# Performance work log

Hardware: AMD Instinct MI355X
Metric: run time of the kernel (lower is better)

Reference implementation:

```python
import jax, jax.numpy as jnp
import numpy as np

K = 512
D = 512
N_D = 4
SUB_D = D // N_D  # 128
B, T = 16, 2048
TAU = 2.0


def setup_inputs() -> dict:
    key = jax.random.key(0)
    kx, kw1, kw2, kw3, kw4, kg = jax.random.split(key, 6)
    x = jax.random.normal(kx, (B, D, T), dtype=jnp.float32)
    scale = 1.0 / K
    def init_w(k):
        return jax.random.uniform(k, (K, SUB_D), dtype=jnp.float32, minval=-scale, maxval=scale)
    W1, W2, W3, W4 = init_w(kw1), init_w(kw2), init_w(kw3), init_w(kw4)
    # Standard Gumbel noise g = -log(-log(U)), fixed here for reproducibility
    u = jax.random.uniform(kg, (N_D, B * T, K), dtype=jnp.float32, minval=1e-10, maxval=1.0)
    gumbels = -jnp.log(-jnp.log(u))
    return {"x": x, "W1": W1, "W2": W2, "W3": W3, "W4": W4, "gumbels": gumbels}


def reference(x, W1, W2, W3, W4, gumbels):
    # x: [B, D, T] -> [B, T, D] -> flat [N, D] -> [n_d, N, sub_D]
    Bv, Dv, Tv = x.shape
    flat = jnp.transpose(x, (0, 2, 1)).reshape(-1, Dv)          # [N, D]
    xg = jnp.transpose(flat.reshape(-1, N_D, SUB_D), (1, 0, 2))  # [n_d, N, sub_D]
    W = jnp.stack([W1, W2, W3, W4], axis=0)                      # [n_d, K, sub_D]

    code_sqr = jnp.sum(W * W, axis=-1)                           # [n_d, K]
    in_sqr = jnp.sum(xg * xg, axis=-1, keepdims=True)            # [n_d, N, 1]
    cross = jnp.einsum('gnd,gkd->gnk', xg, W)                    # [n_d, N, K]
    dis = code_sqr[:, None, :] + in_sqr - 2.0 * cross            # [n_d, N, K]

    # gumbel_softmax(-dis, tau, hard=False): softmax((logits + g)/tau)
    enc = jax.nn.softmax((-dis + gumbels) / TAU, axis=-1)        # [n_d, N, K]

    quant = jnp.einsum('gnk,gkd->gnd', enc, W)                   # [n_d, N, sub_D]
    quant = jnp.transpose(quant, (1, 0, 2)).reshape(Bv, Tv, Dv)  # concat sub-dims
    quant = jnp.transpose(quant, (0, 2, 1))                      # [B, D, T]

    avg_probs = jnp.mean(enc, axis=1)                            # [n_d, K]
    perp = jnp.sum(jnp.exp(-jnp.sum(avg_probs * jnp.log(avg_probs + 1e-10), axis=-1)))
    return quant, perp
```

## Files before the change

kernel.cpp:

```cpp
#include <hip/hip_runtime.h>
#include <hip/hip_bf16.h>
#include <math.h>

#define K_CODES 512
#define D_FULL 512
#define SUB_D 128
#define N_D 4
#define B_SZ 16
#define T_SZ 2048
#define N_TOK (B_SZ * T_SZ)
#define TILE 32
#define QS_STRIDE 33

typedef __attribute__((ext_vector_type(8))) short short8;
typedef __attribute__((ext_vector_type(16))) float f32x16;

__device__ __forceinline__ unsigned short f2bf(float f) {
    __hip_bfloat16 h = __float2bfloat16(f);
    return *reinterpret_cast<unsigned short*>(&h);
}
__device__ __forceinline__ float bf2f(unsigned short u) {
    unsigned int v = ((unsigned int)u) << 16;
    return __uint_as_float(v);
}

#define XS_OFF  32768
#define SMEM_SZ 40960

__device__ __forceinline__ int enc_idx(int r, int c) { return r * 512 + (c ^ ((r & 7) << 3)); }
__device__ __forceinline__ int xs_idx(int t, int d)  { return t * 128 + (d ^ ((t & 7) << 3)); }

__global__ __launch_bounds__(256, 4) void vq_kernel(
    const float* __restrict__ x,
    const unsigned short* __restrict__ Wbf,
    const unsigned short* __restrict__ WTbf,
    const float* __restrict__ csqr,
    const float* __restrict__ gum,
    float* __restrict__ out,
    float* __restrict__ wsum, int Rmask)
{
    __shared__ __align__(16) char smem[SMEM_SZ];
    unsigned short* enc = (unsigned short*)smem;
    unsigned short* xs  = (unsigned short*)(smem + XS_OFF);
    float* Sp   = (float*)smem;
    float* Qs   = (float*)smem;

    const int tid = threadIdx.x;
    const int g = blockIdx.y;
    const int n0 = blockIdx.x * TILE;
    const int b = n0 / T_SZ;
    const int t0 = n0 % T_SZ;
    const int wave = tid >> 6, lane = tid & 63;
    const int half = lane >> 5, l31 = lane & 31;

    const float* xbase = x + ((size_t)b * D_FULL + g * SUB_D) * T_SZ + t0;
    #pragma unroll
    for (int it = 0; it < 4; ++it) {
        int idx = tid + it * 256;
        int tq = idx & 7, d = idx >> 3;
        float4 v = *(const float4*)(xbase + (size_t)d * T_SZ + tq * 4);
        int t = tq * 4;
        xs[xs_idx(t + 0, d)] = f2bf(v.x);
        xs[xs_idx(t + 1, d)] = f2bf(v.y);
        xs[xs_idx(t + 2, d)] = f2bf(v.z);
        xs[xs_idx(t + 3, d)] = f2bf(v.w);
    }
    __syncthreads();

    float csq[4];
    #pragma unroll
    for (int ct = 0; ct < 4; ++ct)
        csq[ct] = csqr[g * K_CODES + wave * 128 + ct * 32 + l31];

    const unsigned short* Wg = Wbf + (size_t)g * K_CODES * SUB_D;
    f32x16 acc[4];
    #pragma unroll
    for (int ct = 0; ct < 4; ++ct)
        #pragma unroll
        for (int i = 0; i < 16; ++i) acc[ct][i] = 0.f;

    #pragma unroll
    for (int s = 0; s < 8; ++s) {
        short8 af = *(const short8*)(xs + xs_idx(l31, s * 16 + half * 8));
        #pragma unroll
        for (int ct = 0; ct < 4; ++ct) {
            short8 bfrag = *(const short8*)(Wg + (size_t)(wave * 128 + ct * 32 + l31) * SUB_D
                                            + s * 16 + half * 8);
            acc[ct] = __builtin_amdgcn_mfma_f32_32x32x16_bf16(af, bfrag, acc[ct], 0, 0, 0);
        }
    }

    __builtin_amdgcn_sched_barrier(0);

    const float* gw = gum + ((size_t)g * N_TOK + n0) * K_CODES + wave * 128;
    float4 f[16];
    #pragma unroll
    for (int k = 0; k < 16; ++k)
        f[k] = *(const float4*)(gw + (size_t)(2 * k + half) * K_CODES + 4 * l31);

    float* Sw = Sp + wave * 544;
    float ssum[16];
    #pragma unroll
    for (int i = 0; i < 16; ++i) ssum[i] = 0.f;

    #pragma unroll
    for (int j = 0; j < 8; ++j) {
        *(float4*)(Sw + half * 128 + 4 * l31)       = f[2 * j];
        *(float4*)(Sw + 256 + half * 128 + 4 * l31) = f[2 * j + 1];
        int hj = j & 1;
        if (half == hj) {
            int q = (j - hj) >> 1;
            #pragma unroll
            for (int ct = 0; ct < 4; ++ct)
                #pragma unroll
                for (int m = 0; m < 4; ++m) {
                    float gv = Sw[m * 128 + ct * 32 + l31];
                    int i = q * 4 + m;
                    float e = __expf(acc[ct][i] - 0.5f * csq[ct] + 0.5f * gv);
                    acc[ct][i] = e;
                    ssum[i] += e;
                }
        }
    }

    #pragma unroll
    for (int i = 0; i < 16; ++i) {
        float s = ssum[i];
        s += __shfl_xor(s, 1);  s += __shfl_xor(s, 2);
        s += __shfl_xor(s, 4);  s += __shfl_xor(s, 8);
        s += __shfl_xor(s, 16);
        ssum[i] = s;
    }
    if (l31 == 0) {
        #pragma unroll
        for (int i = 0; i < 16; ++i)
            Sw[512 + (i & 3) + 8 * (i >> 2) + 4 * half] = ssum[i];
    }
    __syncthreads();

    float rinv[16];
    #pragma unroll
    for (int i = 0; i < 16; ++i) {
        int r = (i & 3) + 8 * (i >> 2) + 4 * half;
        float s = Sp[512 + r] + Sp[544 + 512 + r] + Sp[1088 + 512 + r] + Sp[1632 + 512 + r];
        rinv[i] = 1.f / s;
    }
    __syncthreads();

    float* wrep = wsum + (size_t)(blockIdx.x & Rmask) * (N_D * K_CODES) + g * K_CODES;
    #pragma unroll
    for (int ct = 0; ct < 4; ++ct) {
        float s = 0.f;
        #pragma unroll
        for (int i = 0; i < 16; ++i) {
            int r = (i & 3) + 8 * (i >> 2) + 4 * half;
            float p = acc[ct][i] * rinv[i];
            enc[enc_idx(r, wave * 128 + ct * 32 + l31)] = f2bf(p);
            s += p;
        }
        s += __shfl_xor(s, 32);
        if (half == 0) atomicAdd(wrep + wave * 128 + ct * 32 + l31, s);
    }
    __syncthreads();

    const unsigned short* Btrow = WTbf + (size_t)g * SUB_D * K_CODES
                                + (size_t)(wave * 32 + l31) * K_CODES + half * 8;
    f32x16 q0, q1;
    #pragma unroll
    for (int i = 0; i < 16; ++i) { q0[i] = 0.f; q1[i] = 0.f; }
    #pragma unroll
    for (int s = 0; s < 32; s += 2) {
        short8 a0 = *(const short8*)(enc + enc_idx(l31, (s + 0) * 16 + half * 8));
        short8 b0 = *(const short8*)(Btrow + (s + 0) * 16);
        short8 a1 = *(const short8*)(enc + enc_idx(l31, (s + 1) * 16 + half * 8));
        short8 b1 = *(const short8*)(Btrow + (s + 1) * 16);
        q0 = __builtin_amdgcn_mfma_f32_32x32x16_bf16(a0, b0, q0, 0, 0, 0);
        q1 = __builtin_amdgcn_mfma_f32_32x32x16_bf16(a1, b1, q1, 0, 0, 0);
    }
    __syncthreads();

    #pragma unroll
    for (int i = 0; i < 16; ++i) {
        int r = (i & 3) + 8 * (i >> 2) + 4 * half;
        Qs[(wave * 32 + l31) * QS_STRIDE + r] = q0[i] + q1[i];
    }
    __syncthreads();

    float* obase = out + ((size_t)b * D_FULL + g * SUB_D) * T_SZ + t0;
    #pragma unroll
    for (int it = 0; it < 4; ++it) {
        int idx = tid + it * 256;
        int t4 = (idx & 7) * 4, j = idx >> 3;
        float4 v;
        v.x = Qs[j * QS_STRIDE + t4 + 0];
        v.y = Qs[j * QS_STRIDE + t4 + 1];
        v.z = Qs[j * QS_STRIDE + t4 + 2];
        v.w = Qs[j * QS_STRIDE + t4 + 3];
        *(float4*)(obase + (size_t)j * T_SZ + t4) = v;
    }
}

__global__ __launch_bounds__(256) void prep_kernel(
    const float* __restrict__ W1, const float* __restrict__ W2,
    const float* __restrict__ W3, const float* __restrict__ W4,
    unsigned short* __restrict__ Wbf, unsigned short* __restrict__ WTbf,
    float* __restrict__ csqr)
{
    const int g = blockIdx.x, kc = blockIdx.y;
    const float* Wg = (g == 0) ? W1 : ((g == 1) ? W2 : ((g == 2) ? W3 : W4));
    const int tid = threadIdx.x;
    const int k0 = kc * 64;
    __shared__ float tile[64][129];

    #pragma unroll
    for (int it = 0; it < 8; ++it) {
        int idx = tid + it * 256;
        int k = idx >> 5, d4 = (idx & 31) * 4;
        float4 v = *(const float4*)(Wg + (size_t)(k0 + k) * SUB_D + d4);
        unsigned short p0 = f2bf(v.x), p1 = f2bf(v.y), p2 = f2bf(v.z), p3 = f2bf(v.w);
        tile[k][d4 + 0] = bf2f(p0); tile[k][d4 + 1] = bf2f(p1);
        tile[k][d4 + 2] = bf2f(p2); tile[k][d4 + 3] = bf2f(p3);
        ushort4 pk; pk.x = p0; pk.y = p1; pk.z = p2; pk.w = p3;
        *(ushort4*)(Wbf + (size_t)g * K_CODES * SUB_D + (size_t)(k0 + k) * SUB_D + d4) = pk;
    }
    __syncthreads();

    #pragma unroll
    for (int it = 0; it < 4; ++it) {
        int idx = tid + it * 256;
        int d = idx >> 3, c8 = (idx & 7) * 8;
        union { unsigned short u[8]; short8 v; } pk;
        #pragma unroll
        for (int j = 0; j < 8; ++j) pk.u[j] = f2bf(tile[c8 + j][d]);
        *(short8*)(WTbf + (size_t)g * SUB_D * K_CODES + (size_t)d * K_CODES + k0 + c8) = pk.v;
    }

    if (tid < 64) {
        float ssq = 0.f;
        #pragma unroll 16
        for (int d = 0; d < SUB_D; ++d) { float wv = tile[tid][d]; ssq += wv * wv; }
        csqr[g * K_CODES + k0 + tid] = ssq;
    }
}

__global__ __launch_bounds__(256) void perp_kernel(
    const float* __restrict__ wsum, int R, float* __restrict__ out)
{
    const int tid = threadIdx.x;
    const int lane = tid & 63, wave = tid >> 6;
    __shared__ float red[N_D][4];
    float part[N_D];
    #pragma unroll
    for (int g = 0; g < N_D; ++g) part[g] = 0.f;

    for (int g = 0; g < N_D; ++g) {
        for (int kk = tid; kk < K_CODES; kk += 256) {
            float s = 0.f;
            for (int r = 0; r < R; ++r) s += wsum[(size_t)r * (N_D * K_CODES) + g * K_CODES + kk];
            float p = s * (1.0f / N_TOK);
            part[g] += p * logf(p + 1e-10f);
        }
    }
    #pragma unroll
    for (int g = 0; g < N_D; ++g) {
        float v = part[g];
        #pragma unroll
        for (int off = 32; off; off >>= 1) v += __shfl_xor(v, off);
        if (lane == 0) red[g][wave] = v;
    }
    __syncthreads();
    if (tid == 0) {
        float perp = 0.f;
        #pragma unroll
        for (int g = 0; g < N_D; ++g) {
            float e = red[g][0] + red[g][1] + red[g][2] + red[g][3];
            perp += __expf(-e);
        }
        out[(size_t)B_SZ * D_FULL * T_SZ] = perp;
    }
}

extern "C" void kernel_launch(void* const* d_in, const int* in_sizes, int n_in,
                              void* d_out, int out_size, void* d_ws, size_t ws_size,
                              hipStream_t stream) {
    const float* x   = (const float*)d_in[0];
    const float* W1  = (const float*)d_in[1];
    const float* W2  = (const float*)d_in[2];
    const float* W3  = (const float*)d_in[3];
    const float* W4  = (const float*)d_in[4];
    const float* gum = (const float*)d_in[5];
    float* out = (float*)d_out;

    unsigned short* Wbf  = (unsigned short*)d_ws;
    unsigned short* WTbf = Wbf + (size_t)N_D * K_CODES * SUB_D;
    float* csqr = (float*)(WTbf + (size_t)N_D * K_CODES * SUB_D);
    float* wsum = csqr + N_D * K_CODES;

    size_t fixed = (size_t)N_D * K_CODES * SUB_D * 2 * 2 + (size_t)N_D * K_CODES * 4;
    size_t rem = (ws_size > fixed) ? (ws_size - fixed) : 0;
    int maxR = (int)(rem / ((size_t)N_D * K_CODES * 4));
    int R = 1;
    while (R * 2 <= maxR && R < 16) R *= 2;

    hipMemsetAsync(wsum, 0, (size_t)R * N_D * K_CODES * sizeof(float), stream);
    prep_kernel<<<dim3(4, 8), 256, 0, stream>>>(W1, W2, W3, W4, Wbf, WTbf, csqr);
    vq_kernel<<<dim3(N_TOK / TILE, N_D), 256, 0, stream>>>(x, Wbf, WTbf, csqr, gum, out, wsum, R - 1);
    perp_kernel<<<1, 256, 0, stream>>>(wsum, R, out);
}
```

Baseline: 576.7 us.

## Stream gumbel noise into LDS via async global_load_lds triple buffering

Replaces the register-staged gumbel loads (16 float4 per lane, then written to LDS) with direct global-to-LDS async loads into a three-slot ring per wave. The first loads are issued before the MFMA distance GEMM, so noise fetch overlaps compute, and manual vmcnt waits pace the softmax loop. This lowers register pressure and removes the LDS store pass, but relies on the exact vmcnt ordering and grows per-wave LDS use (1536 floats per wave plus a moved reduction area).

```diff
diff --git a/kernel.cpp b/kernel.cpp
--- a/kernel.cpp
+++ b/kernel.cpp
@@ -1,6 +1,7 @@
 #include <hip/hip_runtime.h>
 #include <hip/hip_bf16.h>
 #include <math.h>
+#include <stdint.h>
 
 #define K_CODES 512
 #define D_FULL 512
@@ -24,8 +25,17 @@
     return __uint_as_float(v);
 }
 
+__device__ __forceinline__ void gld_lds16(const float* g, float* l) {
+    auto gp = reinterpret_cast<const __attribute__((address_space(1))) unsigned int*>(
+        reinterpret_cast<uintptr_t>(g));
+    auto lp = reinterpret_cast<__attribute__((address_space(3))) unsigned int*>(
+        static_cast<unsigned int>(reinterpret_cast<uintptr_t>(l)));
+    __builtin_amdgcn_global_load_lds(gp, lp, 16, 0, 0);
+}
+
 #define XS_OFF  32768
 #define SMEM_SZ 40960
+#define PAD_F   6144
 
 __device__ __forceinline__ int enc_idx(int r, int c) { return r * 512 + (c ^ ((r & 7) << 3)); }
 __device__ __forceinline__ int xs_idx(int t, int d)  { return t * 128 + (d ^ ((t & 7) << 3)); }
@@ -72,6 +82,17 @@
     for (int ct = 0; ct < 4; ++ct)
         csq[ct] = csqr[g * K_CODES + wave * 128 + ct * 32 + l31];
 
+    const float* gw = gum + ((size_t)g * N_TOK + n0) * K_CODES + wave * 128;
+    float* Sw = Sp + wave * 1536;
+
+    #define ISSUE_ROUND(j_) do { \
+        float* dst_ = Sw + ((j_) % 3) * 512; \
+        gld_lds16(gw + (size_t)(4 * (j_) + half) * K_CODES + 4 * l31, dst_); \
+        gld_lds16(gw + (size_t)(4 * (j_) + 2 + half) * K_CODES + 4 * l31, dst_ + 256); \
+    } while (0)
+
+    ISSUE_ROUND(0); ISSUE_ROUND(1); ISSUE_ROUND(2);
+
     const unsigned short* Wg = Wbf + (size_t)g * K_CODES * SUB_D;
     f32x16 acc[4];
     #pragma unroll
@@ -90,38 +111,35 @@
         }
     }
 
-    __builtin_amdgcn_sched_barrier(0);
-
-    const float* gw = gum + ((size_t)g * N_TOK + n0) * K_CODES + wave * 128;
-    float4 f[16];
-    #pragma unroll
-    for (int k = 0; k < 16; ++k)
-        f[k] = *(const float4*)(gw + (size_t)(2 * k + half) * K_CODES + 4 * l31);
-
-    float* Sw = Sp + wave * 544;
     float ssum[16];
     #pragma unroll
     for (int i = 0; i < 16; ++i) ssum[i] = 0.f;
 
     #pragma unroll
     for (int j = 0; j < 8; ++j) {
-        *(float4*)(Sw + half * 128 + 4 * l31)       = f[2 * j];
-        *(float4*)(Sw + 256 + half * 128 + 4 * l31) = f[2 * j + 1];
+        if (j < 6)      asm volatile("s_waitcnt vmcnt(4)" ::: "memory");
+        else if (j == 6) asm volatile("s_waitcnt vmcnt(2)" ::: "memory");
+        else             asm volatile("s_waitcnt vmcnt(0)" ::: "memory");
+        __builtin_amdgcn_sched_barrier(0);
+
         int hj = j & 1;
         if (half == hj) {
-            int q = (j - hj) >> 1;
+            const float* Sb = Sw + (j % 3) * 512;
+            int q = j >> 1;
             #pragma unroll
             for (int ct = 0; ct < 4; ++ct)
                 #pragma unroll
                 for (int m = 0; m < 4; ++m) {
-                    float gv = Sw[m * 128 + ct * 32 + l31];
+                    float gv = Sb[m * 128 + ct * 32 + l31];
                     int i = q * 4 + m;
                     float e = __expf(acc[ct][i] - 0.5f * csq[ct] + 0.5f * gv);
                     acc[ct][i] = e;
                     ssum[i] += e;
                 }
         }
-    }
+        if (j < 5) ISSUE_ROUND(j + 3);
+    }
+    #undef ISSUE_ROUND
 
     #pragma unroll
     for (int i = 0; i < 16; ++i) {
@@ -134,7 +152,7 @@
     if (l31 == 0) {
         #pragma unroll
         for (int i = 0; i < 16; ++i)
-            Sw[512 + (i & 3) + 8 * (i >> 2) + 4 * half] = ssum[i];
+            Sp[PAD_F + wave * 32 + (i & 3) + 8 * (i >> 2) + 4 * half] = ssum[i];
     }
     __syncthreads();
 
@@ -142,7 +160,7 @@
     #pragma unroll
     for (int i = 0; i < 16; ++i) {
         int r = (i & 3) + 8 * (i >> 2) + 4 * half;
-        float s = Sp[512 + r] + Sp[544 + 512 + r] + Sp[1088 + 512 + r] + Sp[1632 + 512 + r];
+        float s = Sp[PAD_F + r] + Sp[PAD_F + 32 + r] + Sp[PAD_F + 64 + r] + Sp[PAD_F + 96 + r];
         rinv[i] = 1.f / s;
     }
     __syncthreads();
```

After: 572.5 us. About the same (-0.7%).
